# Kernel tuning notes

Hardware: AMD Instinct MI355X
Metric: run time of the kernel (lower is better)

## Reference

```python
import jax, jax.numpy as jnp
import numpy as np

N_NODES = 100000


def gcn_conv(x, edge_index, W, b, num_nodes):
    """PyG GCNConv: y = D^{-1/2} (A + I) D^{-1/2} (x W) + b.

    edge_index[0] = source (row), edge_index[1] = target (col);
    messages flow source -> target with symmetric normalization.
    """
    # add self loops
    loop = jnp.arange(num_nodes, dtype=edge_index.dtype)
    row = jnp.concatenate([edge_index[0], loop])  # [E+N]
    col = jnp.concatenate([edge_index[1], loop])  # [E+N]

    xw = x @ W  # [N, F_out] -- tiny GEMM, done before gather

    # degree of target nodes (incl. self loops)
    ones = jnp.ones(col.shape[0], dtype=x.dtype)
    deg = jax.ops.segment_sum(ones, col, num_segments=num_nodes)  # [N]
    dis = jax.lax.rsqrt(jnp.maximum(deg, 1e-12))
    dis = jnp.where(deg > 0, dis, 0.0)

    norm = dis[row] * dis[col]  # [E+N]
    msg = xw[row] * norm[:, None]  # gather + scale, [E+N, F_out]
    out = jax.ops.segment_sum(msg, col, num_segments=num_nodes)  # scatter-add
    return out + b


def setup_inputs() -> dict:
    key = jax.random.key(0)
    k1, k2, k3, k4 = jax.random.split(key, 4)
    num_attr, hidden, num_classes = 128, 16, 8
    n_edges = 3200000
    x = jax.random.normal(k1, (N_NODES, num_attr), dtype=jnp.float32)
    edge_index = jax.random.randint(k2, (2, n_edges), 0, N_NODES, dtype=jnp.int64)
    W1 = jax.random.normal(k3, (num_attr, hidden), dtype=jnp.float32) / np.sqrt(num_attr)
    b1 = jnp.zeros((hidden,), dtype=jnp.float32)
    W2 = jax.random.normal(k4, (hidden, num_classes), dtype=jnp.float32) / np.sqrt(hidden)
    b2 = jnp.zeros((num_classes,), dtype=jnp.float32)
    return {"x": x, "edge_index": edge_index, "W1": W1, "b1": b1, "W2": W2, "b2": b2}


def reference(x, edge_index, W1, b1, W2, b2):
    h = gcn_conv(x, edge_index, W1, b1, N_NODES)
    h = jax.nn.relu(h)
    # dropout is identity in eval mode
    h = gcn_conv(h, edge_index, W2, b2, N_NODES)
    return jax.nn.sigmoid(h)  # [N, num_classes]
```

## Files before the change

### kernel.cpp

```cpp
#include <hip/hip_runtime.h>
#include <math.h>

static constexpr int FI = 128;
static constexpr int FH = 16;
static constexpr int FO = 8;

static constexpr int BIN_SHIFT = 8;
static constexpr int BIN_NODES = 256;
static constexpr int MAX_BINS  = 512;
static constexpr int CAPB      = 8832;
static constexpr int SCHUNK    = 8192;
static constexpr int SThreads  = 512;

__device__ __forceinline__ unsigned short f2bf(float x) {
    unsigned u = __float_as_uint(x);
    u += 0x7FFFu + ((u >> 16) & 1u);
    return (unsigned short)(u >> 16);
}
__device__ __forceinline__ float bflo(unsigned u) { return __uint_as_float(u << 16); }
__device__ __forceinline__ float bfhi(unsigned u) { return __uint_as_float(u & 0xFFFF0000u); }

struct SMemScatter {
    int lcnt[MAX_BINS];
    int lstart[MAX_BINS];
    int lcur[MAX_BINS];
    int gbase[MAX_BINS];
    int wsum[8];
    unsigned int   staged[SCHUNK];
    unsigned short sbin[SCHUNK];
};
struct SMemGemm { float sw[FI * FH]; };
union SMemU { SMemScatter s; SMemGemm g; };

__launch_bounds__(SThreads)
__global__ void k_scatter_gemm(const int* __restrict__ row, const int* __restrict__ col,
                               int* __restrict__ binCursor, unsigned int* __restrict__ binned,
                               const float* __restrict__ x, const float* __restrict__ W1,
                               unsigned short* __restrict__ xw1, int E, int nchunks, int N) {
    __shared__ SMemU sm;
    int t = threadIdx.x;

    if ((int)blockIdx.x >= nchunks) {
        for (int i = t; i < FI * FH; i += SThreads) sm.g.sw[i] = W1[i];
        __syncthreads();
        int nl = t >> 2;
        int f  = (t & 3) * 4;
        int n  = ((int)blockIdx.x - nchunks) * 128 + nl;
        if (n >= N) return;
        const float4* xr = (const float4*)(x + (size_t)n * FI);
        float a0 = 0.f, a1 = 0.f, a2 = 0.f, a3 = 0.f;
        #pragma unroll 8
        for (int kq = 0; kq < FI / 4; ++kq) {
            float4 xv = xr[kq];
            float4 w0 = *(const float4*)&sm.g.sw[(kq * 4 + 0) * FH + f];
            float4 w1 = *(const float4*)&sm.g.sw[(kq * 4 + 1) * FH + f];
            float4 w2 = *(const float4*)&sm.g.sw[(kq * 4 + 2) * FH + f];
            float4 w3 = *(const float4*)&sm.g.sw[(kq * 4 + 3) * FH + f];
            a0 = fmaf(xv.x, w0.x, a0); a1 = fmaf(xv.x, w0.y, a1);
            a2 = fmaf(xv.x, w0.z, a2); a3 = fmaf(xv.x, w0.w, a3);
            a0 = fmaf(xv.y, w1.x, a0); a1 = fmaf(xv.y, w1.y, a1);
            a2 = fmaf(xv.y, w1.z, a2); a3 = fmaf(xv.y, w1.w, a3);
            a0 = fmaf(xv.z, w2.x, a0); a1 = fmaf(xv.z, w2.y, a1);
            a2 = fmaf(xv.z, w2.z, a2); a3 = fmaf(xv.z, w2.w, a3);
            a0 = fmaf(xv.w, w3.x, a0); a1 = fmaf(xv.w, w3.y, a1);
            a2 = fmaf(xv.w, w3.z, a2); a3 = fmaf(xv.w, w3.w, a3);
        }
        unsigned w0 = (unsigned)f2bf(a0) | ((unsigned)f2bf(a1) << 16);
        unsigned w1 = (unsigned)f2bf(a2) | ((unsigned)f2bf(a3) << 16);
        *(uint2*)(xw1 + (size_t)n * FH + f) = make_uint2(w0, w1);
        return;
    }

    int base = blockIdx.x * SCHUNK;
    int end  = base + SCHUNK; if (end > E) end = E;
    int m = end - base;
    sm.s.lcnt[t] = 0;
    __syncthreads();

    int nv = m >> 2;
    const int4* c4 = (const int4*)(col + base);
    int4 creg[4];
    #pragma unroll
    for (int j = 0; j < 4; ++j) {
        int k = t + j * SThreads;
        if (k < nv) {
            creg[j] = c4[k];
            atomicAdd(&sm.s.lcnt[creg[j].x >> BIN_SHIFT], 1);
            atomicAdd(&sm.s.lcnt[creg[j].y >> BIN_SHIFT], 1);
            atomicAdd(&sm.s.lcnt[creg[j].z >> BIN_SHIFT], 1);
            atomicAdd(&sm.s.lcnt[creg[j].w >> BIN_SHIFT], 1);
        }
    }
    for (int i = base + (nv << 2) + t; i < end; i += SThreads)
        atomicAdd(&sm.s.lcnt[col[i] >> BIN_SHIFT], 1);
    __syncthreads();

    int v = sm.s.lcnt[t];
    int inc = v;
    #pragma unroll
    for (int d = 1; d < 64; d <<= 1) {
        int u = __shfl_up(inc, d, 64);
        if ((t & 63) >= d) inc += u;
    }
    if ((t & 63) == 63) sm.s.wsum[t >> 6] = inc;
    __syncthreads();
    if (t < 8) {
        int w = sm.s.wsum[t];
        #pragma unroll
        for (int d = 1; d < 8; d <<= 1) {
            int u = __shfl_up(w, d, 8);
            if (t >= d) w += u;
        }
        sm.s.wsum[t] = w;
    }
    __syncthreads();
    {
        int waveoff = (t >= 64) ? sm.s.wsum[(t >> 6) - 1] : 0;
        int ex = waveoff + inc - v;
        sm.s.lstart[t] = ex;
        sm.s.lcur[t]   = ex;
        sm.s.gbase[t]  = v ? atomicAdd(&binCursor[t], v) : 0;
    }
    __syncthreads();

    const int4* r4 = (const int4*)(row + base);
    #pragma unroll
    for (int j = 0; j < 4; ++j) {
        int k = t + j * SThreads;
        if (k < nv) {
            int4 r = r4[k];
            int cc[4] = {creg[j].x, creg[j].y, creg[j].z, creg[j].w};
            int rr[4] = {r.x, r.y, r.z, r.w};
            #pragma unroll
            for (int jj = 0; jj < 4; ++jj) {
                int b = cc[jj] >> BIN_SHIFT;
                int pos = atomicAdd(&sm.s.lcur[b], 1);
                sm.s.staged[pos] = (unsigned)rr[jj] | ((unsigned)(cc[jj] & (BIN_NODES - 1)) << 17);
                sm.s.sbin[pos] = (unsigned short)b;
            }
        }
    }
    for (int i = base + (nv << 2) + t; i < end; i += SThreads) {
        int c = col[i];
        int b = c >> BIN_SHIFT;
        int pos = atomicAdd(&sm.s.lcur[b], 1);
        sm.s.staged[pos] = (unsigned)row[i] | ((unsigned)(c & (BIN_NODES - 1)) << 17);
        sm.s.sbin[pos] = (unsigned short)b;
    }
    __syncthreads();

    for (int i = t; i < m; i += SThreads) {
        int b = sm.s.sbin[i];
        int off = sm.s.gbase[b] + (i - sm.s.lstart[b]);
        if (off < CAPB) binned[b * CAPB + off] = sm.s.staged[i];
    }
}

__launch_bounds__(BIN_NODES)
__global__ void k_refine(const int* __restrict__ binCursor, const unsigned int* __restrict__ binned,
                         int* __restrict__ srow, int* __restrict__ starts, int* __restrict__ ends,
                         float* __restrict__ dis, unsigned short* __restrict__ xw1, int N) {
    __shared__ unsigned int  stage[CAPB];
    __shared__ unsigned char arr[CAPB];
    __shared__ int cnt[BIN_NODES];
    __shared__ int wsum[4];
    int t = threadIdx.x;
    int b = blockIdx.x;
    int s = b * CAPB;
    int m = binCursor[b];
    if (m > CAPB) m = CAPB;
    cnt[t] = 0;
    __syncthreads();

    int mm = m & ~3;
    for (int i0 = t * 4; i0 < mm; i0 += BIN_NODES * 4) {
        uint4 v = *(const uint4*)(binned + s + i0);
        *(uint4*)&stage[i0] = v;
        arr[i0 + 0] = (unsigned char)atomicAdd(&cnt[v.x >> 17], 1);
        arr[i0 + 1] = (unsigned char)atomicAdd(&cnt[v.y >> 17], 1);
        arr[i0 + 2] = (unsigned char)atomicAdd(&cnt[v.z >> 17], 1);
        arr[i0 + 3] = (unsigned char)atomicAdd(&cnt[v.w >> 17], 1);
    }
    for (int i = mm + t; i < m; i += BIN_NODES) {
        unsigned v = binned[s + i];
        stage[i] = v;
        arr[i] = (unsigned char)atomicAdd(&cnt[v >> 17], 1);
    }
    __syncthreads();

    int deg = cnt[t];
    int inc = deg;
    #pragma unroll
    for (int d = 1; d < 64; d <<= 1) {
        int u = __shfl_up(inc, d, 64);
        if ((t & 63) >= d) inc += u;
    }
    if ((t & 63) == 63) wsum[t >> 6] = inc;
    __syncthreads();
    if (t < 4) {
        int w = wsum[t];
        #pragma unroll
        for (int d = 1; d < 4; d <<= 1) {
            int u = __shfl_up(w, d, 4);
            if (t >= d) w += u;
        }
        wsum[t] = w;
    }
    __syncthreads();
    int waveoff = (t >= 64) ? wsum[(t >> 6) - 1] : 0;
    int excl = waveoff + inc - deg;

    int n = b * BIN_NODES + t;
    float dv = rsqrtf((float)(deg + 1));
    if (n < N) {
        starts[n] = s + excl;
        ends[n]   = s + excl + deg;
        dis[n]    = dv;
    }
    cnt[t] = excl;
    __syncthreads();

    for (int i0 = t * 4; i0 < mm; i0 += BIN_NODES * 4) {
        uint4 v = *(uint4*)&stage[i0];
        srow[s + cnt[v.x >> 17] + arr[i0 + 0]] = v.x & 0x1FFFF;
        srow[s + cnt[v.y >> 17] + arr[i0 + 1]] = v.y & 0x1FFFF;
        srow[s + cnt[v.z >> 17] + arr[i0 + 2]] = v.z & 0x1FFFF;
        srow[s + cnt[v.w >> 17] + arr[i0 + 3]] = v.w & 0x1FFFF;
    }
    for (int i = mm + t; i < m; i += BIN_NODES) {
        unsigned v = stage[i];
        srow[s + cnt[v >> 17] + arr[i]] = v & 0x1FFFF;
    }

    if (n < N) {
        uint4* p = (uint4*)(xw1 + (size_t)n * FH);
        uint4 va = p[0], vb = p[1];
        unsigned* u = &va.x;
        #pragma unroll
        for (int k = 0; k < 4; ++k)
            u[k] = (unsigned)f2bf(bflo(u[k]) * dv) | ((unsigned)f2bf(bfhi(u[k]) * dv) << 16);
        unsigned* w = &vb.x;
        #pragma unroll
        for (int k = 0; k < 4; ++k)
            w[k] = (unsigned)f2bf(bflo(w[k]) * dv) | ((unsigned)f2bf(bfhi(w[k]) * dv) << 16);
        p[0] = va; p[1] = vb;
    }
}

__launch_bounds__(256)
__global__ void k_agg1(const int* __restrict__ starts, const int* __restrict__ ends,
                       const int* __restrict__ srow, const float* __restrict__ dis,
                       const unsigned short* __restrict__ xw1s, const float* __restrict__ W2,
                       const float* __restrict__ b1, unsigned short* __restrict__ xw2s, int N) {
    __shared__ float sw[FH * FO];
    __shared__ float sb[FH];
    int t = threadIdx.x;
    if (t < FH * FO) sw[t] = W2[t];
    if (t < FH) sb[t] = b1[t];
    __syncthreads();

    int n = blockIdx.x * 128 + (t >> 1);
    int h = t & 1;
    if (n >= N) return;
    float dn = dis[n];
    int s = starts[n], e = ends[n];
    const uint4* xq = (const uint4*)xw1s;

    uint4 sp = xq[(size_t)n * 2 + h];
    float acc[8];
    acc[0]=bflo(sp.x); acc[1]=bfhi(sp.x); acc[2]=bflo(sp.y); acc[3]=bfhi(sp.y);
    acc[4]=bflo(sp.z); acc[5]=bfhi(sp.z); acc[6]=bflo(sp.w); acc[7]=bfhi(sp.w);

    int i = s;
    for (; i + 8 <= e; i += 8) {
        int rr[8];
        #pragma unroll
        for (int j = 0; j < 8; ++j) rr[j] = srow[i + j];
        uint4 pk[8];
        #pragma unroll
        for (int j = 0; j < 8; ++j) pk[j] = xq[(size_t)rr[j] * 2 + h];
        #pragma unroll
        for (int j = 0; j < 8; ++j) {
            acc[0]+=bflo(pk[j].x); acc[1]+=bfhi(pk[j].x);
            acc[2]+=bflo(pk[j].y); acc[3]+=bfhi(pk[j].y);
            acc[4]+=bflo(pk[j].z); acc[5]+=bfhi(pk[j].z);
            acc[6]+=bflo(pk[j].w); acc[7]+=bfhi(pk[j].w);
        }
    }
    for (; i < e; ++i) {
        uint4 p = xq[(size_t)srow[i] * 2 + h];
        acc[0]+=bflo(p.x); acc[1]+=bfhi(p.x);
        acc[2]+=bflo(p.y); acc[3]+=bfhi(p.y);
        acc[4]+=bflo(p.z); acc[5]+=bfhi(p.z);
        acc[6]+=bflo(p.w); acc[7]+=bfhi(p.w);
    }

    float hv[8];
    #pragma unroll
    for (int k = 0; k < 8; ++k) {
        float v = fmaf(dn, acc[k], sb[h * 8 + k]);
        hv[k] = v > 0.f ? v : 0.f;
    }
    float po[FO];
    #pragma unroll
    for (int o = 0; o < FO; ++o) {
        float a = 0.f;
        #pragma unroll
        for (int k = 0; k < 8; ++k) a = fmaf(hv[k], sw[(h * 8 + k) * FO + o], a);
        po[o] = a;
    }
    #pragma unroll
    for (int o = 0; o < FO; ++o) po[o] += __shfl_xor(po[o], 1, 64);
    int o0 = h * 4;
    unsigned w0 = (unsigned)f2bf(po[o0 + 0] * dn) | ((unsigned)f2bf(po[o0 + 1] * dn) << 16);
    unsigned w1 = (unsigned)f2bf(po[o0 + 2] * dn) | ((unsigned)f2bf(po[o0 + 3] * dn) << 16);
    *(uint2*)(xw2s + (size_t)n * FO + o0) = make_uint2(w0, w1);
}

__launch_bounds__(256)
__global__ void k_agg2(const int* __restrict__ starts, const int* __restrict__ ends,
                       const int* __restrict__ srow, const float* __restrict__ dis,
                       const unsigned short* __restrict__ xw2s, const float* __restrict__ b2,
                       float* __restrict__ out, int N) {
    int t = threadIdx.x;
    int n = blockIdx.x * 128 + (t >> 1);
    int h = t & 1;
    if (n >= N) return;
    float dn = dis[n];
    int s = starts[n], e = ends[n];
    const uint2* xq = (const uint2*)xw2s;

    uint2 sp = xq[(size_t)n * 2 + h];
    float acc[4];
    acc[0]=bflo(sp.x); acc[1]=bfhi(sp.x); acc[2]=bflo(sp.y); acc[3]=bfhi(sp.y);

    int i = s;
    for (; i + 8 <= e; i += 8) {
        int rr[8];
        #pragma unroll
        for (int j = 0; j < 8; ++j) rr[j] = srow[i + j];
        uint2 pk[8];
        #pragma unroll
        for (int j = 0; j < 8; ++j) pk[j] = xq[(size_t)rr[j] * 2 + h];
        #pragma unroll
        for (int j = 0; j < 8; ++j) {
            acc[0]+=bflo(pk[j].x); acc[1]+=bfhi(pk[j].x);
            acc[2]+=bflo(pk[j].y); acc[3]+=bfhi(pk[j].y);
        }
    }
    for (; i < e; ++i) {
        uint2 p = xq[(size_t)srow[i] * 2 + h];
        acc[0]+=bflo(p.x); acc[1]+=bfhi(p.x);
        acc[2]+=bflo(p.y); acc[3]+=bfhi(p.y);
    }

    int f0 = h * 4;
    float r[4];
    #pragma unroll
    for (int k = 0; k < 4; ++k) {
        float v = fmaf(dn, acc[k], b2[f0 + k]);
        r[k] = 1.f / (1.f + __expf(-v));
    }
    *(float4*)(out + (size_t)n * FO + f0) = make_float4(r[0], r[1], r[2], r[3]);
}

extern "C" void kernel_launch(void* const* d_in, const int* in_sizes, int n_in,
                              void* d_out, int out_size, void* d_ws, size_t ws_size,
                              hipStream_t stream) {
    const float* x  = (const float*)d_in[0];
    const int*   ei = (const int*)d_in[1];
    const float* W1 = (const float*)d_in[2];
    const float* b1 = (const float*)d_in[3];
    const float* W2 = (const float*)d_in[4];
    const float* b2 = (const float*)d_in[5];

    const int N = in_sizes[0] / FI;
    const int E = in_sizes[1] / 2;
    const int* row = ei;
    const int* col = ei + E;
    const int nbins = (N + BIN_NODES - 1) >> BIN_SHIFT;

    const int nchunks = (E + SCHUNK - 1) / SCHUNK;
    const int ngemm   = (N + 127) / 128;

    const size_t NP = 100352;
    const size_t BINSZ = (size_t)nbins * CAPB;
    float* base = (float*)d_ws;
    int*   starts    = (int*)base;
    int*   ends      = (int*)(base + NP);
    float* dis       = base + 2 * NP;
    int*   binCursor = (int*)(base + 3 * NP);
    unsigned int* binned = (unsigned int*)(base + 3 * NP + 1024);
    int*   srow      = (int*)(base + 3 * NP + 1024 + BINSZ);
    unsigned short* xw1s = (unsigned short*)(base + 3 * NP + 1024 + 2 * BINSZ);
    unsigned short* xw2s = (unsigned short*)(base + 3 * NP + 1024 + 2 * BINSZ + NP * 8);
    float* out = (float*)d_out;

    size_t needed = (3 * NP + 1024 + 2 * BINSZ + NP * 12) * 4;
    if (ws_size < needed) return;

    hipMemsetAsync(binCursor, 0, (size_t)nbins * sizeof(int), stream);
    k_scatter_gemm<<<nchunks + ngemm, SThreads, 0, stream>>>(row, col, binCursor, binned,
                                                             x, W1, xw1s, E, nchunks, N);
    k_refine      <<<nbins, BIN_NODES,          0, stream>>>(binCursor, binned, srow, starts, ends, dis, xw1s, N);
    k_agg1        <<<(2 * N + 255) / 256, 256,  0, stream>>>(starts, ends, srow, dis, xw1s, W2, b1, xw2s, N);
    k_agg2        <<<(2 * N + 255) / 256, 256,  0, stream>>>(starts, ends, srow, dis, xw2s, b2, out, N);
}
```

Before: 119.7 us.

## Fuse all GCN stages into one persistent cooperative kernel with grid syncs

```diff
diff --git a/kernel.cpp b/kernel.cpp
--- a/kernel.cpp
+++ b/kernel.cpp
@@ -1,5 +1,8 @@
 #include <hip/hip_runtime.h>
+#include <hip/hip_cooperative_groups.h>
 #include <math.h>
+
+namespace cg = cooperative_groups;
 
 static constexpr int FI = 128;
 static constexpr int FH = 16;
@@ -10,7 +13,7 @@
 static constexpr int MAX_BINS  = 512;
 static constexpr int CAPB      = 8832;
 static constexpr int SCHUNK    = 8192;
-static constexpr int SThreads  = 512;
+static constexpr int NT        = 512;
 
 __device__ __forceinline__ unsigned short f2bf(float x) {
     unsigned u = __float_as_uint(x);
@@ -20,7 +23,7 @@
 __device__ __forceinline__ float bflo(unsigned u) { return __uint_as_float(u << 16); }
 __device__ __forceinline__ float bfhi(unsigned u) { return __uint_as_float(u & 0xFFFF0000u); }
 
-struct SMemScatter {
+struct SScatter {
     int lcnt[MAX_BINS];
     int lstart[MAX_BINS];
     int lcur[MAX_BINS];
@@ -29,339 +32,326 @@
     unsigned int   staged[SCHUNK];
     unsigned short sbin[SCHUNK];
 };
-struct SMemGemm { float sw[FI * FH]; };
-union SMemU { SMemScatter s; SMemGemm g; };
-
-__launch_bounds__(SThreads)
-__global__ void k_scatter_gemm(const int* __restrict__ row, const int* __restrict__ col,
-                               int* __restrict__ binCursor, unsigned int* __restrict__ binned,
-                               const float* __restrict__ x, const float* __restrict__ W1,
-                               unsigned short* __restrict__ xw1, int E, int nchunks, int N) {
-    __shared__ SMemU sm;
-    int t = threadIdx.x;
-
-    if ((int)blockIdx.x >= nchunks) {
-        for (int i = t; i < FI * FH; i += SThreads) sm.g.sw[i] = W1[i];
-        __syncthreads();
-        int nl = t >> 2;
-        int f  = (t & 3) * 4;
-        int n  = ((int)blockIdx.x - nchunks) * 128 + nl;
-        if (n >= N) return;
-        const float4* xr = (const float4*)(x + (size_t)n * FI);
-        float a0 = 0.f, a1 = 0.f, a2 = 0.f, a3 = 0.f;
-        #pragma unroll 8
-        for (int kq = 0; kq < FI / 4; ++kq) {
-            float4 xv = xr[kq];
-            float4 w0 = *(const float4*)&sm.g.sw[(kq * 4 + 0) * FH + f];
-            float4 w1 = *(const float4*)&sm.g.sw[(kq * 4 + 1) * FH + f];
-            float4 w2 = *(const float4*)&sm.g.sw[(kq * 4 + 2) * FH + f];
-            float4 w3 = *(const float4*)&sm.g.sw[(kq * 4 + 3) * FH + f];
-            a0 = fmaf(xv.x, w0.x, a0); a1 = fmaf(xv.x, w0.y, a1);
-            a2 = fmaf(xv.x, w0.z, a2); a3 = fmaf(xv.x, w0.w, a3);
-            a0 = fmaf(xv.y, w1.x, a0); a1 = fmaf(xv.y, w1.y, a1);
-            a2 = fmaf(xv.y, w1.z, a2); a3 = fmaf(xv.y, w1.w, a3);
-            a0 = fmaf(xv.z, w2.x, a0); a1 = fmaf(xv.z, w2.y, a1);
-            a2 = fmaf(xv.z, w2.z, a2); a3 = fmaf(xv.z, w2.w, a3);
-            a0 = fmaf(xv.w, w3.x, a0); a1 = fmaf(xv.w, w3.y, a1);
-            a2 = fmaf(xv.w, w3.z, a2); a3 = fmaf(xv.w, w3.w, a3);
-        }
-        unsigned w0 = (unsigned)f2bf(a0) | ((unsigned)f2bf(a1) << 16);
-        unsigned w1 = (unsigned)f2bf(a2) | ((unsigned)f2bf(a3) << 16);
-        *(uint2*)(xw1 + (size_t)n * FH + f) = make_uint2(w0, w1);
-        return;
+struct SRefine {
+    unsigned char arr[CAPB];
+    int cnt[BIN_NODES];
+    int wsum[4];
+};
+struct SGemm { float sw[FI * FH]; };
+struct SAgg  { float sw[FH * FO]; float sb[FH]; };
+union USm { SScatter s; SRefine r; SGemm g; SAgg a; };
+
+__launch_bounds__(NT, 4)
+__global__ void k_gcn(const int* __restrict__ row, const int* __restrict__ col,
+                      int* __restrict__ binCursor, unsigned int* __restrict__ binned,
+                      int* __restrict__ srow, int* __restrict__ starts,
+                      int* __restrict__ ends, float* __restrict__ dis,
+                      const float* __restrict__ x, const float* __restrict__ W1,
+                      unsigned short* __restrict__ xw1s, const float* __restrict__ W2,
+                      const float* __restrict__ b1, unsigned short* __restrict__ xw2s,
+                      const float* __restrict__ b2, float* __restrict__ out,
+                      int E, int N) {
+    cg::grid_group grid = cg::this_grid();
+    __shared__ USm sm;
+    const int t  = threadIdx.x;
+    const int nb = gridDim.x;
+    const int nbins   = (N + BIN_NODES - 1) >> BIN_SHIFT;
+    const int nchunks = (E + SCHUNK - 1) / SCHUNK;
+    const int ngemm   = (N + 127) >> 7;
+
+    for (int item = blockIdx.x; item < nchunks + ngemm; item += nb) {
+        __syncthreads();
+        if (item < nchunks) {
+            int base = item * SCHUNK;
+            int end  = base + SCHUNK; if (end > E) end = E;
+            int m = end - base;
+            sm.s.lcnt[t] = 0;
+            __syncthreads();
+            int nv = m >> 2;
+            const int4* c4 = (const int4*)(col + base);
+            int4 creg[4];
+            #pragma unroll
+            for (int j = 0; j < 4; ++j) {
+                int k = t + j * NT;
+                if (k < nv) {
+                    creg[j] = c4[k];
+                    atomicAdd(&sm.s.lcnt[creg[j].x >> BIN_SHIFT], 1);
+                    atomicAdd(&sm.s.lcnt[creg[j].y >> BIN_SHIFT], 1);
+                    atomicAdd(&sm.s.lcnt[creg[j].z >> BIN_SHIFT], 1);
+                    atomicAdd(&sm.s.lcnt[creg[j].w >> BIN_SHIFT], 1);
+                }
+            }
+            for (int i = base + (nv << 2) + t; i < end; i += NT)
+                atomicAdd(&sm.s.lcnt[col[i] >> BIN_SHIFT], 1);
+            __syncthreads();
+            int v = sm.s.lcnt[t];
+            int inc = v;
+            #pragma unroll
+            for (int d = 1; d < 64; d <<= 1) {
+                int u = __shfl_up(inc, d, 64);
+                if ((t & 63) >= d) inc += u;
+            }
+            if ((t & 63) == 63) sm.s.wsum[t >> 6] = inc;
+            __syncthreads();
+            if (t < 8) {
+                int w = sm.s.wsum[t];
+                #pragma unroll
+                for (int d = 1; d < 8; d <<= 1) {
+                    int u = __shfl_up(w, d, 8);
+                    if (t >= d) w += u;
+                }
+                sm.s.wsum[t] = w;
+            }
+            __syncthreads();
+            {
+                int waveoff = (t >= 64) ? sm.s.wsum[(t >> 6) - 1] : 0;
+                int ex = waveoff + inc - v;
+                sm.s.lstart[t] = ex;
+                sm.s.lcur[t]   = ex;
+                sm.s.gbase[t]  = v ? atomicAdd(&binCursor[t], v) : 0;
+            }
+            __syncthreads();
+            const int4* r4 = (const int4*)(row + base);
+            #pragma unroll
+            for (int j = 0; j < 4; ++j) {
+                int k = t + j * NT;
+                if (k < nv) {
+                    int4 r = r4[k];
+                    int cc[4] = {creg[j].x, creg[j].y, creg[j].z, creg[j].w};
+                    int rr[4] = {r.x, r.y, r.z, r.w};
+                    #pragma unroll
+                    for (int jj = 0; jj < 4; ++jj) {
+                        int bb = cc[jj] >> BIN_SHIFT;
+                        int pos = atomicAdd(&sm.s.lcur[bb], 1);
+                        sm.s.staged[pos] = (unsigned)rr[jj] | ((unsigned)(cc[jj] & (BIN_NODES - 1)) << 17);
+                        sm.s.sbin[pos] = (unsigned short)bb;
+                    }
+                }
+            }
+            for (int i = base + (nv << 2) + t; i < end; i += NT) {
+                int c = col[i];
+                int bb = c >> BIN_SHIFT;
+                int pos = atomicAdd(&sm.s.lcur[bb], 1);
+                sm.s.staged[pos] = (unsigned)row[i] | ((unsigned)(c & (BIN_NODES - 1)) << 17);
+                sm.s.sbin[pos] = (unsigned short)bb;
+            }
+            __syncthreads();
+            for (int i = t; i < m; i += NT) {
+                int bb = sm.s.sbin[i];
+                int off = sm.s.gbase[bb] + (i - sm.s.lstart[bb]);
+                if (off < CAPB) binned[bb * CAPB + off] = sm.s.staged[i];
+            }
+        } else {
+            int tile = item - nchunks;
+            for (int i = t; i < FI * FH; i += NT) sm.g.sw[i] = W1[i];
+            __syncthreads();
+            int nl = t >> 2;
+            int f  = (t & 3) * 4;
+            int n  = tile * 128 + nl;
+            if (n < N) {
+                const float4* xr = (const float4*)(x + (size_t)n * FI);
+                float a0 = 0.f, a1 = 0.f, a2 = 0.f, a3 = 0.f;
+                #pragma unroll 8
+                for (int kq = 0; kq < FI / 4; ++kq) {
+                    float4 xv = xr[kq];
+                    float4 w0 = *(const float4*)&sm.g.sw[(kq * 4 + 0) * FH + f];
+                    float4 w1 = *(const float4*)&sm.g.sw[(kq * 4 + 1) * FH + f];
+                    float4 w2 = *(const float4*)&sm.g.sw[(kq * 4 + 2) * FH + f];
+                    float4 w3 = *(const float4*)&sm.g.sw[(kq * 4 + 3) * FH + f];
+                    a0 = fmaf(xv.x, w0.x, a0); a1 = fmaf(xv.x, w0.y, a1);
+                    a2 = fmaf(xv.x, w0.z, a2); a3 = fmaf(xv.x, w0.w, a3);
+                    a0 = fmaf(xv.y, w1.x, a0); a1 = fmaf(xv.y, w1.y, a1);
+                    a2 = fmaf(xv.y, w1.z, a2); a3 = fmaf(xv.y, w1.w, a3);
+                    a0 = fmaf(xv.z, w2.x, a0); a1 = fmaf(xv.z, w2.y, a1);
+                    a2 = fmaf(xv.z, w2.z, a2); a3 = fmaf(xv.z, w2.w, a3);
+                    a0 = fmaf(xv.w, w3.x, a0); a1 = fmaf(xv.w, w3.y, a1);
+                    a2 = fmaf(xv.w, w3.z, a2); a3 = fmaf(xv.w, w3.w, a3);
+                }
+                unsigned p0 = (unsigned)f2bf(a0) | ((unsigned)f2bf(a1) << 16);
+                unsigned p1 = (unsigned)f2bf(a2) | ((unsigned)f2bf(a3) << 16);
+                *(uint2*)(xw1s + (size_t)n * FH + f) = make_uint2(p0, p1);
+            }
+        }
     }
-
-    int base = blockIdx.x * SCHUNK;
-    int end  = base + SCHUNK; if (end > E) end = E;
-    int m = end - base;
-    sm.s.lcnt[t] = 0;
+    grid.sync();
+
+    for (int b = blockIdx.x; b < nbins; b += nb) {
+        __syncthreads();
+        int s = b * CAPB;
+        int m = binCursor[b]; if (m > CAPB) m = CAPB;
+        if (t < BIN_NODES) sm.r.cnt[t] = 0;
+        __syncthreads();
+        int mm = m & ~3;
+        for (int i0 = t * 4; i0 < mm; i0 += NT * 4) {
+            uint4 v = *(const uint4*)(binned + s + i0);
+            sm.r.arr[i0 + 0] = (unsigned char)atomicAdd(&sm.r.cnt[v.x >> 17], 1);
+            sm.r.arr[i0 + 1] = (unsigned char)atomicAdd(&sm.r.cnt[v.y >> 17], 1);
+            sm.r.arr[i0 + 2] = (unsigned char)atomicAdd(&sm.r.cnt[v.z >> 17], 1);
+            sm.r.arr[i0 + 3] = (unsigned char)atomicAdd(&sm.r.cnt[v.w >> 17], 1);
+        }
+        for (int i = mm + t; i < m; i += NT)
+            sm.r.arr[i] = (unsigned char)atomicAdd(&sm.r.cnt[binned[s + i] >> 17], 1);
+        __syncthreads();
+        int deg = 0, inc = 0;
+        if (t < BIN_NODES) {
+            deg = sm.r.cnt[t]; inc = deg;
+            #pragma unroll
+            for (int d = 1; d < 64; d <<= 1) {
+                int u = __shfl_up(inc, d, 64);
+                if ((t & 63) >= d) inc += u;
+            }
+            if ((t & 63) == 63) sm.r.wsum[t >> 6] = inc;
+        }
+        __syncthreads();
+        if (t < 4) {
+            int w = sm.r.wsum[t];
+            #pragma unroll
+            for (int d = 1; d < 4; d <<= 1) {
+                int u = __shfl_up(w, d, 4);
+                if (t >= d) w += u;
+            }
+            sm.r.wsum[t] = w;
+        }
+        __syncthreads();
+        if (t < BIN_NODES) {
+            int waveoff = (t >= 64) ? sm.r.wsum[(t >> 6) - 1] : 0;
+            int excl = waveoff + inc - deg;
+            int n = b * BIN_NODES + t;
+            float dv = rsqrtf((float)(deg + 1));
+            if (n < N) {
+                starts[n] = s + excl;
+                ends[n]   = s + excl + deg;
+                dis[n]    = dv;
+                uint4* p = (uint4*)(xw1s + (size_t)n * FH);
+                uint4 va = p[0], vb = p[1];
+                unsigned* ua = &va.x;
+                #pragma unroll
+                for (int k = 0; k < 4; ++k)
+                    ua[k] = (unsigned)f2bf(bflo(ua[k]) * dv) | ((unsigned)f2bf(bfhi(ua[k]) * dv) << 16);
+                unsigned* ub = &vb.x;
+                #pragma unroll
+                for (int k = 0; k < 4; ++k)
+                    ub[k] = (unsigned)f2bf(bflo(ub[k]) * dv) | ((unsigned)f2bf(bfhi(ub[k]) * dv) << 16);
+                p[0] = va; p[1] = vb;
+            }
+            sm.r.cnt[t] = excl;
+        }
+        __syncthreads();
+        for (int i0 = t * 4; i0 < mm; i0 += NT * 4) {
+            uint4 v = *(const uint4*)(binned + s + i0);
+            srow[s + sm.r.cnt[v.x >> 17] + sm.r.arr[i0 + 0]] = v.x & 0x1FFFF;
+            srow[s + sm.r.cnt[v.y >> 17] + sm.r.arr[i0 + 1]] = v.y & 0x1FFFF;
+            srow[s + sm.r.cnt[v.z >> 17] + sm.r.arr[i0 + 2]] = v.z & 0x1FFFF;
+            srow[s + sm.r.cnt[v.w >> 17] + sm.r.arr[i0 + 3]] = v.w & 0x1FFFF;
+        }
+        for (int i = mm + t; i < m; i += NT) {
+            unsigned v = binned[s + i];
+            srow[s + sm.r.cnt[v >> 17] + sm.r.arr[i]] = v & 0x1FFFF;
+        }
+    }
+    grid.sync();
+
     __syncthreads();
-
-    int nv = m >> 2;
-    const int4* c4 = (const int4*)(col + base);
-    int4 creg[4];
-    #pragma unroll
-    for (int j = 0; j < 4; ++j) {
-        int k = t + j * SThreads;
-        if (k < nv) {
-            creg[j] = c4[k];
-            atomicAdd(&sm.s.lcnt[creg[j].x >> BIN_SHIFT], 1);
-            atomicAdd(&sm.s.lcnt[creg[j].y >> BIN_SHIFT], 1);
-            atomicAdd(&sm.s.lcnt[creg[j].z >> BIN_SHIFT], 1);
-            atomicAdd(&sm.s.lcnt[creg[j].w >> BIN_SHIFT], 1);
-        }
+    if (t < FH * FO) sm.a.sw[t] = W2[t];
+    if (t < FH) sm.a.sb[t] = b1[t];
+    __syncthreads();
+    for (int L = blockIdx.x * NT + t; L < 2 * N; L += nb * NT) {
+        int n = L >> 1, h = L & 1;
+        float dn = dis[n];
+        int s = starts[n], e = ends[n];
+        const uint4* xq = (const uint4*)xw1s;
+
+        uint4 sp = xq[(size_t)n * 2 + h];
+        float acc[8];
+        acc[0]=bflo(sp.x); acc[1]=bfhi(sp.x); acc[2]=bflo(sp.y); acc[3]=bfhi(sp.y);
+        acc[4]=bflo(sp.z); acc[5]=bfhi(sp.z); acc[6]=bflo(sp.w); acc[7]=bfhi(sp.w);
+
+        int i = s;
+        for (; i + 8 <= e; i += 8) {
+            int rr[8];
+            #pragma unroll
+            for (int j = 0; j < 8; ++j) rr[j] = srow[i + j];
+            uint4 pk[8];
+            #pragma unroll
+            for (int j = 0; j < 8; ++j) pk[j] = xq[(size_t)rr[j] * 2 + h];
+            #pragma unroll
+            for (int j = 0; j < 8; ++j) {
+                acc[0]+=bflo(pk[j].x); acc[1]+=bfhi(pk[j].x);
+                acc[2]+=bflo(pk[j].y); acc[3]+=bfhi(pk[j].y);
+                acc[4]+=bflo(pk[j].z); acc[5]+=bfhi(pk[j].z);
+                acc[6]+=bflo(pk[j].w); acc[7]+=bfhi(pk[j].w);
+            }
+        }
+        for (; i < e; ++i) {
+            uint4 p = xq[(size_t)srow[i] * 2 + h];
+            acc[0]+=bflo(p.x); acc[1]+=bfhi(p.x);
+            acc[2]+=bflo(p.y); acc[3]+=bfhi(p.y);
+            acc[4]+=bflo(p.z); acc[5]+=bfhi(p.z);
+            acc[6]+=bflo(p.w); acc[7]+=bfhi(p.w);
+        }
+
+        float hv[8];
+        #pragma unroll
+        for (int k = 0; k < 8; ++k) {
+            float v = fmaf(dn, acc[k], sm.a.sb[h * 8 + k]);
+            hv[k] = v > 0.f ? v : 0.f;
+        }
+        float po[FO];
+        #pragma unroll
+        for (int o = 0; o < FO; ++o) {
+            float a = 0.f;
+            #pragma unroll
+            for (int k = 0; k < 8; ++k) a = fmaf(hv[k], sm.a.sw[(h * 8 + k) * FO + o], a);
+            po[o] = a;
+        }
+        #pragma unroll
+        for (int o = 0; o < FO; ++o) po[o] += __shfl_xor(po[o], 1, 64);
+        int o0 = h * 4;
+        unsigned q0 = (unsigned)f2bf(po[o0 + 0] * dn) | ((unsigned)f2bf(po[o0 + 1] * dn) << 16);
+        unsigned q1 = (unsigned)f2bf(po[o0 + 2] * dn) | ((unsigned)f2bf(po[o0 + 3] * dn) << 16);
+        *(uint2*)(xw2s + (size_t)n * FO + o0) = make_uint2(q0, q1);
     }
-    for (int i = base + (nv << 2) + t; i < end; i += SThreads)
-        atomicAdd(&sm.s.lcnt[col[i] >> BIN_SHIFT], 1);
-    __syncthreads();
-
-    int v = sm.s.lcnt[t];
-    int inc = v;
-    #pragma unroll
-    for (int d = 1; d < 64; d <<= 1) {
-        int u = __shfl_up(inc, d, 64);
-        if ((t & 63) >= d) inc += u;
+    grid.sync();
+
+    for (int L = blockIdx.x * NT + t; L < 2 * N; L += nb * NT) {
+        int n = L >> 1, h = L & 1;
+        float dn = dis[n];
+        int s = starts[n], e = ends[n];
+        const uint2* xq = (const uint2*)xw2s;
+
+        uint2 sp = xq[(size_t)n * 2 + h];
+        float acc[4];
+        acc[0]=bflo(sp.x); acc[1]=bfhi(sp.x); acc[2]=bflo(sp.y); acc[3]=bfhi(sp.y);
+
+        int i = s;
+        for (; i + 8 <= e; i += 8) {
+            int rr[8];
+            #pragma unroll
+            for (int j = 0; j < 8; ++j) rr[j] = srow[i + j];
+            uint2 pk[8];
+            #pragma unroll
+            for (int j = 0; j < 8; ++j) pk[j] = xq[(size_t)rr[j] * 2 + h];
+            #pragma unroll
+            for (int j = 0; j < 8; ++j) {
+                acc[0]+=bflo(pk[j].x); acc[1]+=bfhi(pk[j].x);
+                acc[2]+=bflo(pk[j].y); acc[3]+=bfhi(pk[j].y);
+            }
+        }
+        for (; i < e; ++i) {
+            uint2 p = xq[(size_t)srow[i] * 2 + h];
+            acc[0]+=bflo(p.x); acc[1]+=bfhi(p.x);
+            acc[2]+=bflo(p.y); acc[3]+=bfhi(p.y);
+        }
+
+        int f0 = h * 4;
+        float r[4];
+        #pragma unroll
+        for (int k = 0; k < 4; ++k) {
+            float v = fmaf(dn, acc[k], b2[f0 + k]);
+            r[k] = 1.f / (1.f + __expf(-v));
+        }
+        *(float4*)(out + (size_t)n * FO + f0) = make_float4(r[0], r[1], r[2], r[3]);
     }
-    if ((t & 63) == 63) sm.s.wsum[t >> 6] = inc;
-    __syncthreads();
-    if (t < 8) {
-        int w = sm.s.wsum[t];
-        #pragma unroll
-        for (int d = 1; d < 8; d <<= 1) {
-            int u = __shfl_up(w, d, 8);
-            if (t >= d) w += u;
-        }
-        sm.s.wsum[t] = w;
-    }
-    __syncthreads();
-    {
-        int waveoff = (t >= 64) ? sm.s.wsum[(t >> 6) - 1] : 0;
-        int ex = waveoff + inc - v;
-        sm.s.lstart[t] = ex;
-        sm.s.lcur[t]   = ex;
-        sm.s.gbase[t]  = v ? atomicAdd(&binCursor[t], v) : 0;
-    }
-    __syncthreads();
-
-    const int4* r4 = (const int4*)(row + base);
-    #pragma unroll
-    for (int j = 0; j < 4; ++j) {
-        int k = t + j * SThreads;
-        if (k < nv) {
-            int4 r = r4[k];
-            int cc[4] = {creg[j].x, creg[j].y, creg[j].z, creg[j].w};
-            int rr[4] = {r.x, r.y, r.z, r.w};
-            #pragma unroll
-            for (int jj = 0; jj < 4; ++jj) {
-                int b = cc[jj] >> BIN_SHIFT;
-                int pos = atomicAdd(&sm.s.lcur[b], 1);
-                sm.s.staged[pos] = (unsigned)rr[jj] | ((unsigned)(cc[jj] & (BIN_NODES - 1)) << 17);
-                sm.s.sbin[pos] = (unsigned short)b;
-            }
-        }
-    }
-    for (int i = base + (nv << 2) + t; i < end; i += SThreads) {
-        int c = col[i];
-        int b = c >> BIN_SHIFT;
-        int pos = atomicAdd(&sm.s.lcur[b], 1);
-        sm.s.staged[pos] = (unsigned)row[i] | ((unsigned)(c & (BIN_NODES - 1)) << 17);
-        sm.s.sbin[pos] = (unsigned short)b;
-    }
-    __syncthreads();
-
-    for (int i = t; i < m; i += SThreads) {
-        int b = sm.s.sbin[i];
-        int off = sm.s.gbase[b] + (i - sm.s.lstart[b]);
-        if (off < CAPB) binned[b * CAPB + off] = sm.s.staged[i];
-    }
-}
-
-__launch_bounds__(BIN_NODES)
-__global__ void k_refine(const int* __restrict__ binCursor, const unsigned int* __restrict__ binned,
-                         int* __restrict__ srow, int* __restrict__ starts, int* __restrict__ ends,
-                         float* __restrict__ dis, unsigned short* __restrict__ xw1, int N) {
-    __shared__ unsigned int  stage[CAPB];
-    __shared__ unsigned char arr[CAPB];
-    __shared__ int cnt[BIN_NODES];
-    __shared__ int wsum[4];
-    int t = threadIdx.x;
-    int b = blockIdx.x;
-    int s = b * CAPB;
-    int m = binCursor[b];
-    if (m > CAPB) m = CAPB;
-    cnt[t] = 0;
-    __syncthreads();
-
-    int mm = m & ~3;
-    for (int i0 = t * 4; i0 < mm; i0 += BIN_NODES * 4) {
-        uint4 v = *(const uint4*)(binned + s + i0);
-        *(uint4*)&stage[i0] = v;
-        arr[i0 + 0] = (unsigned char)atomicAdd(&cnt[v.x >> 17], 1);
-        arr[i0 + 1] = (unsigned char)atomicAdd(&cnt[v.y >> 17], 1);
-        arr[i0 + 2] = (unsigned char)atomicAdd(&cnt[v.z >> 17], 1);
-        arr[i0 + 3] = (unsigned char)atomicAdd(&cnt[v.w >> 17], 1);
-    }
-    for (int i = mm + t; i < m; i += BIN_NODES) {
-        unsigned v = binned[s + i];
-        stage[i] = v;
-        arr[i] = (unsigned char)atomicAdd(&cnt[v >> 17], 1);
-    }
-    __syncthreads();
-
-    int deg = cnt[t];
-    int inc = deg;
-    #pragma unroll
-    for (int d = 1; d < 64; d <<= 1) {
-        int u = __shfl_up(inc, d, 64);
-        if ((t & 63) >= d) inc += u;
-    }
-    if ((t & 63) == 63) wsum[t >> 6] = inc;
-    __syncthreads();
-    if (t < 4) {
-        int w = wsum[t];
-        #pragma unroll
-        for (int d = 1; d < 4; d <<= 1) {
-            int u = __shfl_up(w, d, 4);
-            if (t >= d) w += u;
-        }
-        wsum[t] = w;
-    }
-    __syncthreads();
-    int waveoff = (t >= 64) ? wsum[(t >> 6) - 1] : 0;
-    int excl = waveoff + inc - deg;
-
-    int n = b * BIN_NODES + t;
-    float dv = rsqrtf((float)(deg + 1));
-    if (n < N) {
-        starts[n] = s + excl;
-        ends[n]   = s + excl + deg;
-        dis[n]    = dv;
-    }
-    cnt[t] = excl;
-    __syncthreads();
-
-    for (int i0 = t * 4; i0 < mm; i0 += BIN_NODES * 4) {
-        uint4 v = *(uint4*)&stage[i0];
-        srow[s + cnt[v.x >> 17] + arr[i0 + 0]] = v.x & 0x1FFFF;
-        srow[s + cnt[v.y >> 17] + arr[i0 + 1]] = v.y & 0x1FFFF;
-        srow[s + cnt[v.z >> 17] + arr[i0 + 2]] = v.z & 0x1FFFF;
-        srow[s + cnt[v.w >> 17] + arr[i0 + 3]] = v.w & 0x1FFFF;
-    }
-    for (int i = mm + t; i < m; i += BIN_NODES) {
-        unsigned v = stage[i];
-        srow[s + cnt[v >> 17] + arr[i]] = v & 0x1FFFF;
-    }
-
-    if (n < N) {
-        uint4* p = (uint4*)(xw1 + (size_t)n * FH);
-        uint4 va = p[0], vb = p[1];
-        unsigned* u = &va.x;
-        #pragma unroll
-        for (int k = 0; k < 4; ++k)
-            u[k] = (unsigned)f2bf(bflo(u[k]) * dv) | ((unsigned)f2bf(bfhi(u[k]) * dv) << 16);
-        unsigned* w = &vb.x;
-        #pragma unroll
-        for (int k = 0; k < 4; ++k)
-            w[k] = (unsigned)f2bf(bflo(w[k]) * dv) | ((unsigned)f2bf(bfhi(w[k]) * dv) << 16);
-        p[0] = va; p[1] = vb;
-    }
-}
-
-__launch_bounds__(256)
-__global__ void k_agg1(const int* __restrict__ starts, const int* __restrict__ ends,
-                       const int* __restrict__ srow, const float* __restrict__ dis,
-                       const unsigned short* __restrict__ xw1s, const float* __restrict__ W2,
-                       const float* __restrict__ b1, unsigned short* __restrict__ xw2s, int N) {
-    __shared__ float sw[FH * FO];
-    __shared__ float sb[FH];
-    int t = threadIdx.x;
-    if (t < FH * FO) sw[t] = W2[t];
-    if (t < FH) sb[t] = b1[t];
-    __syncthreads();
-
-    int n = blockIdx.x * 128 + (t >> 1);
-    int h = t & 1;
-    if (n >= N) return;
-    float dn = dis[n];
-    int s = starts[n], e = ends[n];
-    const uint4* xq = (const uint4*)xw1s;
-
-    uint4 sp = xq[(size_t)n * 2 + h];
-    float acc[8];
-    acc[0]=bflo(sp.x); acc[1]=bfhi(sp.x); acc[2]=bflo(sp.y); acc[3]=bfhi(sp.y);
-    acc[4]=bflo(sp.z); acc[5]=bfhi(sp.z); acc[6]=bflo(sp.w); acc[7]=bfhi(sp.w);
-
-    int i = s;
-    for (; i + 8 <= e; i += 8) {
-        int rr[8];
-        #pragma unroll
-        for (int j = 0; j < 8; ++j) rr[j] = srow[i + j];
-        uint4 pk[8];
-        #pragma unroll
-        for (int j = 0; j < 8; ++j) pk[j] = xq[(size_t)rr[j] * 2 + h];
-        #pragma unroll
-        for (int j = 0; j < 8; ++j) {
-            acc[0]+=bflo(pk[j].x); acc[1]+=bfhi(pk[j].x);
-            acc[2]+=bflo(pk[j].y); acc[3]+=bfhi(pk[j].y);
-            acc[4]+=bflo(pk[j].z); acc[5]+=bfhi(pk[j].z);
-            acc[6]+=bflo(pk[j].w); acc[7]+=bfhi(pk[j].w);
-        }
-    }
-    for (; i < e; ++i) {
-        uint4 p = xq[(size_t)srow[i] * 2 + h];
-        acc[0]+=bflo(p.x); acc[1]+=bfhi(p.x);
-        acc[2]+=bflo(p.y); acc[3]+=bfhi(p.y);
-        acc[4]+=bflo(p.z); acc[5]+=bfhi(p.z);
-        acc[6]+=bflo(p.w); acc[7]+=bfhi(p.w);
-    }
-
-    float hv[8];
-    #pragma unroll
-    for (int k = 0; k < 8; ++k) {
-        float v = fmaf(dn, acc[k], sb[h * 8 + k]);
-        hv[k] = v > 0.f ? v : 0.f;
-    }
-    float po[FO];
-    #pragma unroll
-    for (int o = 0; o < FO; ++o) {
-        float a = 0.f;
-        #pragma unroll
-        for (int k = 0; k < 8; ++k) a = fmaf(hv[k], sw[(h * 8 + k) * FO + o], a);
-        po[o] = a;
-    }
-    #pragma unroll
-    for (int o = 0; o < FO; ++o) po[o] += __shfl_xor(po[o], 1, 64);
-    int o0 = h * 4;
-    unsigned w0 = (unsigned)f2bf(po[o0 + 0] * dn) | ((unsigned)f2bf(po[o0 + 1] * dn) << 16);
-    unsigned w1 = (unsigned)f2bf(po[o0 + 2] * dn) | ((unsigned)f2bf(po[o0 + 3] * dn) << 16);
-    *(uint2*)(xw2s + (size_t)n * FO + o0) = make_uint2(w0, w1);
-}
-
-__launch_bounds__(256)
-__global__ void k_agg2(const int* __restrict__ starts, const int* __restrict__ ends,
-                       const int* __restrict__ srow, const float* __restrict__ dis,
-                       const unsigned short* __restrict__ xw2s, const float* __restrict__ b2,
-                       float* __restrict__ out, int N) {
-    int t = threadIdx.x;
-    int n = blockIdx.x * 128 + (t >> 1);
-    int h = t & 1;
-    if (n >= N) return;
-    float dn = dis[n];
-    int s = starts[n], e = ends[n];
-    const uint2* xq = (const uint2*)xw2s;
-
-    uint2 sp = xq[(size_t)n * 2 + h];
-    float acc[4];
-    acc[0]=bflo(sp.x); acc[1]=bfhi(sp.x); acc[2]=bflo(sp.y); acc[3]=bfhi(sp.y);
-
-    int i = s;
-    for (; i + 8 <= e; i += 8) {
-        int rr[8];
-        #pragma unroll
-        for (int j = 0; j < 8; ++j) rr[j] = srow[i + j];
-        uint2 pk[8];
-        #pragma unroll
-        for (int j = 0; j < 8; ++j) pk[j] = xq[(size_t)rr[j] * 2 + h];
-        #pragma unroll
-        for (int j = 0; j < 8; ++j) {
-            acc[0]+=bflo(pk[j].x); acc[1]+=bfhi(pk[j].x);
-            acc[2]+=bflo(pk[j].y); acc[3]+=bfhi(pk[j].y);
-        }
-    }
-    for (; i < e; ++i) {
-        uint2 p = xq[(size_t)srow[i] * 2 + h];
-        acc[0]+=bflo(p.x); acc[1]+=bfhi(p.x);
-        acc[2]+=bflo(p.y); acc[3]+=bfhi(p.y);
-    }
-
-    int f0 = h * 4;
-    float r[4];
-    #pragma unroll
-    for (int k = 0; k < 4; ++k) {
-        float v = fmaf(dn, acc[k], b2[f0 + k]);
-        r[k] = 1.f / (1.f + __expf(-v));
-    }
-    *(float4*)(out + (size_t)n * FO + f0) = make_float4(r[0], r[1], r[2], r[3]);
 }
 
 extern "C" void kernel_launch(void* const* d_in, const int* in_sizes, int n_in,
@@ -374,14 +364,11 @@
     const float* W2 = (const float*)d_in[4];
     const float* b2 = (const float*)d_in[5];
 
-    const int N = in_sizes[0] / FI;
-    const int E = in_sizes[1] / 2;
+    int N = in_sizes[0] / FI;
+    int E = in_sizes[1] / 2;
     const int* row = ei;
     const int* col = ei + E;
     const int nbins = (N + BIN_NODES - 1) >> BIN_SHIFT;
-
-    const int nchunks = (E + SCHUNK - 1) / SCHUNK;
-    const int ngemm   = (N + 127) / 128;
 
     const size_t NP = 100352;
     const size_t BINSZ = (size_t)nbins * CAPB;
@@ -399,10 +386,24 @@
     size_t needed = (3 * NP + 1024 + 2 * BINSZ + NP * 12) * 4;
     if (ws_size < needed) return;
 
+    int dev = 0;
+    hipGetDevice(&dev);
+    int numCU = 256;
+    hipDeviceGetAttribute(&numCU, hipDeviceAttributeMultiprocessorCount, dev);
+    int maxB = 0;
+    hipOccupancyMaxActiveBlocksPerMultiprocessor(&maxB, k_gcn, NT, 0);
+    if (maxB < 1) maxB = 1;
+    long long grid = (long long)maxB * numCU;
+    const int nchunks = (E + SCHUNK - 1) / SCHUNK;
+    const int ngemm   = (N + 127) >> 7;
+    if (grid > (long long)(nchunks + ngemm)) grid = nchunks + ngemm;
+    if (grid < 1) grid = 1;
+
     hipMemsetAsync(binCursor, 0, (size_t)nbins * sizeof(int), stream);
-    k_scatter_gemm<<<nchunks + ngemm, SThreads, 0, stream>>>(row, col, binCursor, binned,
-                                                             x, W1, xw1s, E, nchunks, N);
-    k_refine      <<<nbins, BIN_NODES,          0, stream>>>(binCursor, binned, srow, starts, ends, dis, xw1s, N);
-    k_agg1        <<<(2 * N + 255) / 256, 256,  0, stream>>>(starts, ends, srow, dis, xw1s, W2, b1, xw2s, N);
-    k_agg2        <<<(2 * N + 255) / 256, 256,  0, stream>>>(starts, ends, srow, dis, xw2s, b2, out, N);
+
+    void* args[] = { (void*)&row, (void*)&col, (void*)&binCursor, (void*)&binned,
+                     (void*)&srow, (void*)&starts, (void*)&ends, (void*)&dis,
+                     (void*)&x, (void*)&W1, (void*)&xw1s, (void*)&W2, (void*)&b1,
+                     (void*)&xw2s, (void*)&b2, (void*)&out, (void*)&E, (void*)&N };
+    hipLaunchCooperativeKernel((void*)k_gcn, dim3((unsigned)grid), dim3(NT), args, 0, stream);
 }
```

Measured after the change: 242.3 us. 2.02x slower.
